# Kernel tuning notes

Hardware: AMD Instinct MI355X
Metric: run time of the kernel (lower is better)

Reference implementation:

```python
import jax, jax.numpy as jnp
import numpy as np

N = 100000   # nodes
E = 1600000  # edges
HID = 128    # hidden_dim
H = 8        # heads
C = HID // H # head_dim = out_channels per head


def setup_inputs() -> dict:
    key = jax.random.key(0)
    ks = jax.random.split(key, 10)
    x = jax.random.normal(ks[0], (N, HID), jnp.float32)
    edge_index = jax.random.randint(ks[1], (2, E), 0, N, dtype=jnp.int64)
    edge_attr = jax.random.uniform(ks[2], (E,), jnp.float32)
    # GATConv params (lin_src == lin_dst shared since in_channels is int)
    W = jax.random.normal(ks[3], (HID, H * C), jnp.float32) / np.sqrt(HID)
    att_src = jax.random.normal(ks[4], (H, C), jnp.float32) / np.sqrt(C)
    att_dst = jax.random.normal(ks[5], (H, C), jnp.float32) / np.sqrt(C)
    # lin_edge: Linear(edge_dim=1, H*C, bias=False) -> weight [H*C, 1] stored as [H, C]
    w_edge = jax.random.normal(ks[6], (H, C), jnp.float32)
    att_edge = jax.random.normal(ks[7], (H, C), jnp.float32) / np.sqrt(C)
    bias = jnp.zeros((H * C,), jnp.float32)
    gamma = jnp.ones((HID,), jnp.float32)
    beta = jnp.zeros((HID,), jnp.float32)
    return dict(x=x, edge_index=edge_index, edge_attr=edge_attr, W=W,
                att_src=att_src, att_dst=att_dst, w_edge=w_edge,
                att_edge=att_edge, bias=bias, gamma=gamma, beta=beta)


def reference(x, edge_index, edge_attr, W, att_src, att_dst, w_edge, att_edge, bias, gamma, beta):
    n = x.shape[0]
    src, dst = edge_index[0], edge_index[1]
    # add_self_loops with fill_value='mean': loop edge_attr = per-dst-node mean of edge_attr
    ones = jnp.ones_like(edge_attr)
    deg = jax.ops.segment_sum(ones, dst, num_segments=n)
    loop_attr = jax.ops.segment_sum(edge_attr, dst, num_segments=n) / jnp.maximum(deg, 1.0)
    ar = jnp.arange(n, dtype=src.dtype)
    src = jnp.concatenate([src, ar])
    dst = jnp.concatenate([dst, ar])
    ea = jnp.concatenate([edge_attr, loop_attr])  # [E+N]

    h = (x @ W).reshape(n, H, C)                  # [N,H,C]
    a_src = (h * att_src).sum(-1)                 # [N,H]
    a_dst = (h * att_dst).sum(-1)                 # [N,H]
    # edge_dim=1: alpha_edge = <lin_edge(ea), att_edge> = ea * sum(w_edge*att_edge)
    w_e = (w_edge * att_edge).sum(-1)             # [H]
    alpha = a_src[src] + a_dst[dst] + ea[:, None] * w_e  # [E+N, H]
    alpha = jax.nn.leaky_relu(alpha, 0.2)
    # segment softmax over incoming edges of each dst node (all nodes have a self-loop)
    m = jax.ops.segment_max(alpha, dst, num_segments=n)      # [N,H]
    ex = jnp.exp(alpha - m[dst])
    denom = jax.ops.segment_sum(ex, dst, num_segments=n)     # [N,H]
    p = ex / (denom[dst] + 1e-16)
    # scatter-aggregate weighted messages, concat heads, bias
    out = jax.ops.segment_sum(p[:, :, None] * h[src], dst, num_segments=n)
    out = out.reshape(n, H * C) + bias
    # residual + LayerNorm + ReLU
    y = out + x
    mu = y.mean(-1, keepdims=True)
    var = ((y - mu) ** 2).mean(-1, keepdims=True)
    y = (y - mu) * jax.lax.rsqrt(var + 1e-5) * gamma + beta
    return jax.nn.relu(y)
```

## Files before the change

kernel.cpp:

```cpp
#include <hip/hip_runtime.h>
#include <math.h>

#define HID 128
#define HEADS 8
#define CDIM 16
#define BKT 256
#define SCATB 512
#define SCAP 3136

typedef short bf8 __attribute__((ext_vector_type(8)));
typedef float f32x4 __attribute__((ext_vector_type(4)));
typedef float f32x2 __attribute__((ext_vector_type(2)));

__device__ __forceinline__ unsigned short f2bf(float f) {
    unsigned u = __float_as_uint(f);
    unsigned r = (u + 0x7fffu + ((u >> 16) & 1u)) >> 16;
    return (unsigned short)r;
}
__device__ __forceinline__ float bf2f(unsigned short u) {
    return __uint_as_float(((unsigned)u) << 16);
}

__global__ __launch_bounds__(256) void k_tw(const float* __restrict__ W,
                                            unsigned short* __restrict__ Wt,
                                            int* __restrict__ btot,
                                            int* __restrict__ bcur, int nbkt) {
    int idx = blockIdx.x * 256 + threadIdx.x;
    if (idx < HID * HID) {
        int j = idx >> 7, k = idx & 127;
        Wt[idx] = f2bf(W[k * HID + j]);
    }
    if (idx < nbkt) { btot[idx] = 0; bcur[idx] = 0; }
}

__global__ __launch_bounds__(256) void k_hist(const int* __restrict__ dst,
                                              int* __restrict__ btot,
                                              int E, int per, int nbkt) {
    __shared__ int h[512];
    int t = threadIdx.x;
    for (int b = t; b < nbkt; b += 256) h[b] = 0;
    __syncthreads();
    int b0 = blockIdx.x * per;
    int b1 = min(b0 + per, E);
    for (int e = b0 + t; e < b1; e += 256)
        atomicAdd(&h[dst[e] >> 8], 1);
    __syncthreads();
    for (int b = t; b < nbkt; b += 256)
        if (h[b]) atomicAdd(&btot[b], h[b]);
}

__global__ __launch_bounds__(512) void k_scan(const int* __restrict__ btot,
                                              int* __restrict__ bbase, int nbkt,
                                              const float* __restrict__ w_edge,
                                              const float* __restrict__ att_edge,
                                              float* __restrict__ w_e) {
    __shared__ int lds[512];
    int t = threadIdx.x;
    if (t < HEADS) {
        float s = 0.f;
        for (int c = 0; c < CDIM; c++) s += w_edge[t * CDIM + c] * att_edge[t * CDIM + c];
        w_e[t] = s;
    }
    lds[t] = (t < nbkt) ? btot[t] : 0;
    __syncthreads();
    for (int off = 1; off < 512; off <<= 1) {
        int xv = (t >= off) ? lds[t - off] : 0;
        __syncthreads();
        lds[t] += xv;
        __syncthreads();
    }
    if (t < nbkt) bbase[t] = t ? lds[t - 1] : 0;
    if (t == nbkt) bbase[t] = lds[nbkt - 1];
}

__global__ __launch_bounds__(256) void k_mid(const float* __restrict__ x,
                                             const unsigned short* __restrict__ Wt,
                                             const float* __restrict__ att_src,
                                             const float* __restrict__ att_dst,
                                             unsigned short* __restrict__ hbf,
                                             float* __restrict__ a_src,
                                             float* __restrict__ a_dst,
                                             const int* __restrict__ src,
                                             const int* __restrict__ dst,
                                             const float* __restrict__ eattr,
                                             const int* __restrict__ bbase,
                                             int* __restrict__ bcur,
                                             int2* __restrict__ erec1,
                                             int N, int E, int per, int nbkt) {
    if ((int)blockIdx.x < SCATB) {
        __shared__ int2 stg[SCAP];
        __shared__ unsigned short sbkt[SCAP];
        __shared__ int h[512];
        __shared__ int scn[512];
        __shared__ int gB[512];
        __shared__ int cur[512];
        int t = threadIdx.x;
        for (int b = t; b < 512; b += 256) h[b] = 0;
        __syncthreads();
        int b0 = blockIdx.x * per, b1 = min(b0 + per, E);
        for (int e = b0 + t; e < b1; e += 256)
            atomicAdd(&h[dst[e] >> 8], 1);
        __syncthreads();
        scn[t] = h[t];
        scn[t + 256] = h[t + 256];
        __syncthreads();
        for (int off = 1; off < 512; off <<= 1) {
            int x0 = (t >= off) ? scn[t - off] : 0;
            int x1 = (t + 256 >= off) ? scn[t + 256 - off] : 0;
            __syncthreads();
            scn[t] += x0;
            scn[t + 256] += x1;
            __syncthreads();
        }
        for (int b = t; b < nbkt; b += 256) {
            int locB = b ? scn[b - 1] : 0;
            int c = h[b];
            int base = bbase[b];
            if (c) base += atomicAdd(&bcur[b], c);
            gB[b] = base - locB;
            cur[b] = locB;
        }
        __syncthreads();
        for (int e = b0 + t; e < b1; e += 256) {
            int d = dst[e];
            int bb = d >> 8;
            int p = atomicAdd(&cur[bb], 1);
            stg[p] = make_int2((src[e] << 8) | (d & 255), __float_as_int(eattr[e]));
            sbkt[p] = (unsigned short)bb;
        }
        __syncthreads();
        int cnt = b1 - b0;
        for (int p = t; p < cnt; p += 256)
            erec1[gB[sbkt[p]] + p] = stg[p];
        return;
    }
    int tile = blockIdx.x - SCATB;
    int tid = threadIdx.x;
    int wv = tid >> 6, lane = tid & 63;
    int nloc = lane & 15, q = lane >> 4;
    int node = tile * 64 + wv * 16 + nloc;
    int nc = min(node, N - 1);
    const float* xp = x + (size_t)nc * HID + q * 8;
    const unsigned short* wp = Wt + nloc * HID + q * 8;
    f32x4 acc[8];
#pragma unroll
    for (int i = 0; i < 8; i++) acc[i] = (f32x4){0.f, 0.f, 0.f, 0.f};
#pragma unroll
    for (int ch = 0; ch < 4; ch++) {
        float4 xv0 = *(const float4*)(xp + ch * 32);
        float4 xv1 = *(const float4*)(xp + ch * 32 + 4);
        bf8 bfrag;
        bfrag[0] = (short)f2bf(xv0.x); bfrag[1] = (short)f2bf(xv0.y);
        bfrag[2] = (short)f2bf(xv0.z); bfrag[3] = (short)f2bf(xv0.w);
        bfrag[4] = (short)f2bf(xv1.x); bfrag[5] = (short)f2bf(xv1.y);
        bfrag[6] = (short)f2bf(xv1.z); bfrag[7] = (short)f2bf(xv1.w);
#pragma unroll
        for (int jt = 0; jt < 8; jt++) {
            bf8 afrag = *(const bf8*)(wp + (size_t)jt * 16 * HID + ch * 32);
            acc[jt] = __builtin_amdgcn_mfma_f32_16x16x32_bf16(afrag, bfrag, acc[jt], 0, 0, 0);
        }
    }
    bool ok = node < N;
    size_t hb = (size_t)nc * HID;
#pragma unroll
    for (int jt = 0; jt < 8; jt++) {
        int j0 = jt * 16 + q * 4;
        float4 as4 = *(const float4*)(att_src + j0);
        float4 ad4 = *(const float4*)(att_dst + j0);
        f32x4 a = acc[jt];
        float ps = a[0] * as4.x + a[1] * as4.y + a[2] * as4.z + a[3] * as4.w;
        float pd = a[0] * ad4.x + a[1] * ad4.y + a[2] * ad4.z + a[3] * ad4.w;
        ps += __shfl_xor(ps, 16, 64); ps += __shfl_xor(ps, 32, 64);
        pd += __shfl_xor(pd, 16, 64); pd += __shfl_xor(pd, 32, 64);
        if (ok) {
            ushort4 hv;
            hv.x = f2bf(a[0]); hv.y = f2bf(a[1]); hv.z = f2bf(a[2]); hv.w = f2bf(a[3]);
            *(ushort4*)(hbf + hb + j0) = hv;
            if (q == 0) {
                a_src[(size_t)node * 8 + jt] = ps;
                a_dst[(size_t)node * 8 + jt] = pd;
            }
        }
    }
}

__global__ __launch_bounds__(256) void k_bin2(const int* __restrict__ bbase,
                                              const int2* __restrict__ erec1,
                                              int2* __restrict__ erec,
                                              int* __restrict__ row_ptr,
                                              int N, int nbkt) {
    __shared__ int h[256];
    __shared__ int s[256];
    __shared__ int cur[256];
    int b = blockIdx.x, t = threadIdx.x;
    int base = bbase[b], end = bbase[b + 1];
    h[t] = 0;
    __syncthreads();
    for (int e = base + t; e < end; e += 256)
        atomicAdd(&h[erec1[e].x & 255], 1);
    __syncthreads();
    s[t] = h[t];
    __syncthreads();
    for (int off = 1; off < 256; off <<= 1) {
        int v = (t >= off) ? s[t - off] : 0;
        __syncthreads();
        s[t] += v;
        __syncthreads();
    }
    int exc = (t > 0) ? s[t - 1] : 0;
    int node = (b << 8) + t;
    if (node <= N) row_ptr[node] = base + exc;
    cur[t] = base + exc;
    __syncthreads();
    for (int e = base + t; e < end; e += 256) {
        int2 r = erec1[e];
        int pos = atomicAdd(&cur[r.x & 255], 1);
        erec[pos] = make_int2(r.x & 0xFFFFFF00, r.y);
    }
}

__global__ __launch_bounds__(256) void k_node(const int* __restrict__ row_ptr,
                                              const int2* __restrict__ erec,
                                              const float* __restrict__ a_src,
                                              const float* __restrict__ a_dst,
                                              const float* __restrict__ w_e,
                                              const unsigned short* __restrict__ hbf,
                                              const float* __restrict__ x,
                                              const float* __restrict__ bias,
                                              const float* __restrict__ gamma,
                                              const float* __restrict__ beta,
                                              float* __restrict__ out, int N) {
    int wv = threadIdx.x >> 6;
    int lane = threadIdx.x & 63;
    int n = blockIdx.x * 4 + wv;
    if (n >= N) return;
    int r0 = row_ptr[n], r1 = row_ptr[n + 1];
    int sub = lane >> 4;
    int colg = lane & 15;
    int wh = colg >> 1;
    float ad_h = a_dst[(size_t)n * 8 + wh];
    float we_h = w_e[wh];
    const char* hbfc = (const char*)hbf + colg * 16;
    const char* asw  = (const char*)(a_src + wh);

    f32x2 acc2[4];
#pragma unroll
    for (int j = 0; j < 4; j++) acc2[j] = (f32x2){0.f, 0.f};
    float wsum = 0.f, suma = 0.f;
    int rlast = max(r1 - 1, 0);

    for (int eb = r0 + (sub << 2); eb < r1; eb += 16) {
        int e1 = min(eb + 1, rlast);
        int e2 = min(eb + 2, rlast);
        int e3 = min(eb + 3, rlast);
        int2 rec0 = erec[eb];
        int2 rec1 = erec[e1];
        int2 rec2 = erec[e2];
        int2 rec3 = erec[e3];
        bool m1 = (eb + 1) < r1, m2 = (eb + 2) < r1, m3 = (eb + 3) < r1;
        bf8 hv0 = *(const bf8*)(hbfc + rec0.x);
        bf8 hv1 = *(const bf8*)(hbfc + rec1.x);
        bf8 hv2 = *(const bf8*)(hbfc + rec2.x);
        bf8 hv3 = *(const bf8*)(hbfc + rec3.x);
        float as0 = *(const float*)(asw + (rec0.x >> 3));
        float as1 = *(const float*)(asw + (rec1.x >> 3));
        float as2 = *(const float*)(asw + (rec2.x >> 3));
        float as3 = *(const float*)(asw + (rec3.x >> 3));
        float ae0 = __int_as_float(rec0.y);
        float ae1 = __int_as_float(rec1.y);
        float ae2 = __int_as_float(rec2.y);
        float ae3 = __int_as_float(rec3.y);
        float v0 = as0 + ad_h + ae0 * we_h;
        float v1 = as1 + ad_h + ae1 * we_h;
        float v2 = as2 + ad_h + ae2 * we_h;
        float v3 = as3 + ad_h + ae3 * we_h;
        v0 = v0 > 0.f ? v0 : 0.2f * v0;
        v1 = v1 > 0.f ? v1 : 0.2f * v1;
        v2 = v2 > 0.f ? v2 : 0.2f * v2;
        v3 = v3 > 0.f ? v3 : 0.2f * v3;
        float w0 = __expf(v0);
        float w1 = m1 ? __expf(v1) : 0.f;
        float w2 = m2 ? __expf(v2) : 0.f;
        float w3 = m3 ? __expf(v3) : 0.f;
        wsum += (w0 + w1) + (w2 + w3);
        if (colg == 0)
            suma += ae0 + (m1 ? ae1 : 0.f) + (m2 ? ae2 : 0.f) + (m3 ? ae3 : 0.f);
        f32x2 w0v = (f32x2){w0, w0};
        f32x2 w1v = (f32x2){w1, w1};
        f32x2 w2v = (f32x2){w2, w2};
        f32x2 w3v = (f32x2){w3, w3};
#pragma unroll
        for (int j = 0; j < 4; j++) {
            f32x2 h0; h0[0] = bf2f((unsigned short)hv0[2 * j]); h0[1] = bf2f((unsigned short)hv0[2 * j + 1]);
            f32x2 h1; h1[0] = bf2f((unsigned short)hv1[2 * j]); h1[1] = bf2f((unsigned short)hv1[2 * j + 1]);
            f32x2 h2; h2[0] = bf2f((unsigned short)hv2[2 * j]); h2[1] = bf2f((unsigned short)hv2[2 * j + 1]);
            f32x2 h3; h3[0] = bf2f((unsigned short)hv3[2 * j]); h3[1] = bf2f((unsigned short)hv3[2 * j + 1]);
#if __has_builtin(__builtin_elementwise_fma)
            acc2[j] = __builtin_elementwise_fma(w0v, h0, acc2[j]);
            acc2[j] = __builtin_elementwise_fma(w1v, h1, acc2[j]);
            acc2[j] = __builtin_elementwise_fma(w2v, h2, acc2[j]);
            acc2[j] = __builtin_elementwise_fma(w3v, h3, acc2[j]);
#else
            acc2[j][0] = fmaf(w0, h0[0], acc2[j][0]); acc2[j][1] = fmaf(w0, h0[1], acc2[j][1]);
            acc2[j][0] = fmaf(w1, h1[0], acc2[j][0]); acc2[j][1] = fmaf(w1, h1[1], acc2[j][1]);
            acc2[j][0] = fmaf(w2, h2[0], acc2[j][0]); acc2[j][1] = fmaf(w2, h2[1], acc2[j][1]);
            acc2[j][0] = fmaf(w3, h3[0], acc2[j][0]); acc2[j][1] = fmaf(w3, h3[1], acc2[j][1]);
#endif
        }
    }

#pragma unroll
    for (int j = 0; j < 4; j++) {
        acc2[j][0] += __shfl_xor(acc2[j][0], 16, 64);
        acc2[j][0] += __shfl_xor(acc2[j][0], 32, 64);
        acc2[j][1] += __shfl_xor(acc2[j][1], 16, 64);
        acc2[j][1] += __shfl_xor(acc2[j][1], 32, 64);
    }
    wsum += __shfl_xor(wsum, 16, 64);
    wsum += __shfl_xor(wsum, 32, 64);
    suma += __shfl_xor(suma, 16, 64);
    suma += __shfl_xor(suma, 32, 64);

    float accA = sub == 0 ? acc2[0][0] : sub == 1 ? acc2[1][0] : sub == 2 ? acc2[2][0] : acc2[3][0];
    float accB = sub == 0 ? acc2[0][1] : sub == 1 ? acc2[1][1] : sub == 2 ? acc2[2][1] : acc2[3][1];
    int srcL = ((lane & 3) << 4) | (lane >> 2);
    float a0 = __shfl(accA, srcL, 64);
    float a1 = __shfl(accB, srcL, 64);
    int head = lane >> 3;
    float denom = __shfl(wsum, head << 1, 64);
    float sa = __shfl(suma, 0, 64);

    int deg = r1 - r0;
    float la = sa / fmaxf((float)deg, 1.0f);
    float adh = a_dst[(size_t)n * 8 + head];
    float weh = w_e[head];
    float vs = a_src[(size_t)n * 8 + head] + adh + la * weh;
    vs = vs > 0.f ? vs : 0.2f * vs;
    float exs = __expf(vs);
    size_t bx = (size_t)n * HID;
    ushort2 hs = *(const ushort2*)(hbf + bx + 2 * lane);
    a0 = fmaf(exs, bf2f(hs.x), a0);
    a1 = fmaf(exs, bf2f(hs.y), a1);
    float inv = 1.f / (denom + exs + 1e-16f);

    float2 xv = *(const float2*)(x + bx + 2 * lane);
    float2 bv = *(const float2*)(bias + 2 * lane);
    float y0 = a0 * inv + bv.x + xv.x;
    float y1 = a1 * inv + bv.y + xv.y;
    float ss = y0 + y1, sq = y0 * y0 + y1 * y1;
#pragma unroll
    for (int off = 32; off; off >>= 1) {
        ss += __shfl_xor(ss, off, 64);
        sq += __shfl_xor(sq, off, 64);
    }
    float mu = ss * (1.f / 128.f);
    float var = sq * (1.f / 128.f) - mu * mu;
    float r = rsqrtf(fmaxf(var, 0.f) + 1e-5f);
    float2 gv = *(const float2*)(gamma + 2 * lane);
    float2 tv = *(const float2*)(beta + 2 * lane);
    float o0 = (y0 - mu) * r * gv.x + tv.x;
    float o1 = (y1 - mu) * r * gv.y + tv.y;
    float2 ov = make_float2(fmaxf(o0, 0.f), fmaxf(o1, 0.f));
    *(float2*)(out + bx + 2 * lane) = ov;
}

extern "C" void kernel_launch(void* const* d_in, const int* in_sizes, int n_in,
                              void* d_out, int out_size, void* d_ws, size_t ws_size,
                              hipStream_t stream) {
    const float* x        = (const float*)d_in[0];
    const int*   ei       = (const int*)d_in[1];
    const float* eattr    = (const float*)d_in[2];
    const float* W        = (const float*)d_in[3];
    const float* att_src  = (const float*)d_in[4];
    const float* att_dst  = (const float*)d_in[5];
    const float* w_edge   = (const float*)d_in[6];
    const float* att_edge = (const float*)d_in[7];
    const float* bias     = (const float*)d_in[8];
    const float* gamma    = (const float*)d_in[9];
    const float* beta     = (const float*)d_in[10];

    int N = in_sizes[0] / HID;
    int E = in_sizes[2];
    const int* src = ei;
    const int* dst = ei + E;
    float* out = (float*)d_out;

    int nbkt = (N + BKT - 1) / BKT;

    char* ws = (char*)d_ws;
    size_t off = 0;
    auto alloc = [&](size_t bytes) { char* p = ws + off; off += (bytes + 255) & ~255ull; return p; };
    unsigned short* hbf = (unsigned short*)alloc((size_t)N * HID * 2);
    unsigned short* Wt  = (unsigned short*)alloc((size_t)HID * HID * 2);
    float* a_src   = (float*)alloc((size_t)N * 8 * 4);
    float* a_dst   = (float*)alloc((size_t)N * 8 * 4);
    int2*  erec    = (int2*) alloc((size_t)E * 8);
    int2*  erec1   = (int2*) alloc((size_t)E * 8);
    int*   btot    = (int*)  alloc(512 * 4);
    int*   bcur    = (int*)  alloc(512 * 4);
    int*   bbase   = (int*)  alloc(520 * 4);
    int*   row_ptr = (int*)  alloc((size_t)(N + 1) * 4);
    float* w_e     = (float*)alloc(8 * 4);

    int histB = 512;
    int per = (E + histB - 1) / histB;
    int gemmB = (N + 63) / 64;

    k_tw<<<64, 256, 0, stream>>>(W, Wt, btot, bcur, nbkt);
    k_hist<<<histB, 256, 0, stream>>>(dst, btot, E, per, nbkt);
    k_scan<<<1, 512, 0, stream>>>(btot, bbase, nbkt, w_edge, att_edge, w_e);
    k_mid<<<SCATB + gemmB, 256, 0, stream>>>(
        x, Wt, att_src, att_dst, hbf, a_src, a_dst,
        src, dst, eattr, bbase, bcur, erec1, N, E, per, nbkt);
    k_bin2<<<nbkt, 256, 0, stream>>>(bbase, erec1, erec, row_ptr, N, nbkt);
    k_node<<<(N + 3) / 4, 256, 0, stream>>>(row_ptr, erec, a_src, a_dst, w_e, hbf, x,
                                            bias, gamma, beta, out, N);
}
```

Measured before the change: 303.0 us.

## Map one node per 16-lane group and drop global histogram atomics

The node kernel now gives each 16-lane group its own destination node, processing edges two at a time serially, instead of spreading one node's edges across a whole wavefront. That removes the cross-subgroup shuffle reductions and lets the LayerNorm reduce over 16 lanes with float4 loads and stores, at the cost of more per-lane serial work and load imbalance across nodes of different degree. The histogram kernel also takes over the W transpose and writes per-block bucket counts to a matrix rather than using global atomics. The scan sums that matrix and zeroes the cursors, which removes one kernel launch.

```diff
diff --git a/kernel.cpp b/kernel.cpp
--- a/kernel.cpp
+++ b/kernel.cpp
@@ -5,6 +5,8 @@
 #define HEADS 8
 #define CDIM 16
 #define BKT 256
+#define HISTB 256
+#define NBSTR 392
 #define SCATB 512
 #define SCAP 3136
 
@@ -21,36 +23,31 @@
     return __uint_as_float(((unsigned)u) << 16);
 }
 
-__global__ __launch_bounds__(256) void k_tw(const float* __restrict__ W,
-                                            unsigned short* __restrict__ Wt,
-                                            int* __restrict__ btot,
-                                            int* __restrict__ bcur, int nbkt) {
-    int idx = blockIdx.x * 256 + threadIdx.x;
-    if (idx < HID * HID) {
+__global__ __launch_bounds__(256) void k_hist(const float* __restrict__ W,
+                                              unsigned short* __restrict__ Wt,
+                                              const int* __restrict__ dst,
+                                              int* __restrict__ btotmat,
+                                              int E, int per, int nbkt) {
+    __shared__ int h[512];
+    int t = threadIdx.x, bid = blockIdx.x;
+    if (bid < 64) {
+        int idx = bid * 256 + t;
         int j = idx >> 7, k = idx & 127;
         Wt[idx] = f2bf(W[k * HID + j]);
     }
-    if (idx < nbkt) { btot[idx] = 0; bcur[idx] = 0; }
-}
-
-__global__ __launch_bounds__(256) void k_hist(const int* __restrict__ dst,
-                                              int* __restrict__ btot,
-                                              int E, int per, int nbkt) {
-    __shared__ int h[512];
-    int t = threadIdx.x;
-    for (int b = t; b < nbkt; b += 256) h[b] = 0;
-    __syncthreads();
-    int b0 = blockIdx.x * per;
-    int b1 = min(b0 + per, E);
+    h[t] = 0; h[t + 256] = 0;
+    __syncthreads();
+    int b0 = bid * per, b1 = min(b0 + per, E);
     for (int e = b0 + t; e < b1; e += 256)
         atomicAdd(&h[dst[e] >> 8], 1);
     __syncthreads();
     for (int b = t; b < nbkt; b += 256)
-        if (h[b]) atomicAdd(&btot[b], h[b]);
-}
-
-__global__ __launch_bounds__(512) void k_scan(const int* __restrict__ btot,
-                                              int* __restrict__ bbase, int nbkt,
+        btotmat[bid * NBSTR + b] = h[b];
+}
+
+__global__ __launch_bounds__(512) void k_scan(const int* __restrict__ btotmat,
+                                              int* __restrict__ bbase,
+                                              int* __restrict__ bcur, int nbkt,
                                               const float* __restrict__ w_edge,
                                               const float* __restrict__ att_edge,
                                               float* __restrict__ w_e) {
@@ -61,7 +58,11 @@
         for (int c = 0; c < CDIM; c++) s += w_edge[t * CDIM + c] * att_edge[t * CDIM + c];
         w_e[t] = s;
     }
-    lds[t] = (t < nbkt) ? btot[t] : 0;
+    bcur[t] = 0;
+    int sum = 0;
+    if (t < nbkt)
+        for (int i = 0; i < HISTB; i++) sum += btotmat[i * NBSTR + t];
+    lds[t] = sum;
     __syncthreads();
     for (int off = 1; off < 512; off <<= 1) {
         int xv = (t >= off) ? lds[t - off] : 0;
@@ -232,136 +233,114 @@
                                               float* __restrict__ out, int N) {
     int wv = threadIdx.x >> 6;
     int lane = threadIdx.x & 63;
-    int n = blockIdx.x * 4 + wv;
-    if (n >= N) return;
-    int r0 = row_ptr[n], r1 = row_ptr[n + 1];
-    int sub = lane >> 4;
-    int colg = lane & 15;
-    int wh = colg >> 1;
-    float ad_h = a_dst[(size_t)n * 8 + wh];
+    int grp = lane >> 4;
+    int g = lane & 15;
+    int n = (blockIdx.x * 4 + wv) * 4 + grp;
+    bool act = n < N;
+    int nc = act ? n : (N - 1);
+    int r0 = row_ptr[nc], r1 = row_ptr[nc + 1];
+    int wh = g >> 1;
+    float ad_h = a_dst[(size_t)nc * 8 + wh];
     float we_h = w_e[wh];
-    const char* hbfc = (const char*)hbf + colg * 16;
+    const char* hbfc = (const char*)hbf + g * 16;
     const char* asw  = (const char*)(a_src + wh);
 
     f32x2 acc2[4];
 #pragma unroll
     for (int j = 0; j < 4; j++) acc2[j] = (f32x2){0.f, 0.f};
     float wsum = 0.f, suma = 0.f;
-    int rlast = max(r1 - 1, 0);
-
-    for (int eb = r0 + (sub << 2); eb < r1; eb += 16) {
-        int e1 = min(eb + 1, rlast);
-        int e2 = min(eb + 2, rlast);
-        int e3 = min(eb + 3, rlast);
-        int2 rec0 = erec[eb];
+    int rlast = max(r1 - 1, r0);
+
+    for (int e = r0; e < r1; e += 2) {
+        int e1 = min(e + 1, rlast);
+        int2 rec0 = erec[e];
         int2 rec1 = erec[e1];
-        int2 rec2 = erec[e2];
-        int2 rec3 = erec[e3];
-        bool m1 = (eb + 1) < r1, m2 = (eb + 2) < r1, m3 = (eb + 3) < r1;
+        bool m1 = (e + 1) < r1;
         bf8 hv0 = *(const bf8*)(hbfc + rec0.x);
         bf8 hv1 = *(const bf8*)(hbfc + rec1.x);
-        bf8 hv2 = *(const bf8*)(hbfc + rec2.x);
-        bf8 hv3 = *(const bf8*)(hbfc + rec3.x);
         float as0 = *(const float*)(asw + (rec0.x >> 3));
         float as1 = *(const float*)(asw + (rec1.x >> 3));
-        float as2 = *(const float*)(asw + (rec2.x >> 3));
-        float as3 = *(const float*)(asw + (rec3.x >> 3));
         float ae0 = __int_as_float(rec0.y);
         float ae1 = __int_as_float(rec1.y);
-        float ae2 = __int_as_float(rec2.y);
-        float ae3 = __int_as_float(rec3.y);
         float v0 = as0 + ad_h + ae0 * we_h;
         float v1 = as1 + ad_h + ae1 * we_h;
-        float v2 = as2 + ad_h + ae2 * we_h;
-        float v3 = as3 + ad_h + ae3 * we_h;
         v0 = v0 > 0.f ? v0 : 0.2f * v0;
         v1 = v1 > 0.f ? v1 : 0.2f * v1;
-        v2 = v2 > 0.f ? v2 : 0.2f * v2;
-        v3 = v3 > 0.f ? v3 : 0.2f * v3;
         float w0 = __expf(v0);
         float w1 = m1 ? __expf(v1) : 0.f;
-        float w2 = m2 ? __expf(v2) : 0.f;
-        float w3 = m3 ? __expf(v3) : 0.f;
-        wsum += (w0 + w1) + (w2 + w3);
-        if (colg == 0)
-            suma += ae0 + (m1 ? ae1 : 0.f) + (m2 ? ae2 : 0.f) + (m3 ? ae3 : 0.f);
+        wsum += w0 + w1;
+        suma += ae0 + (m1 ? ae1 : 0.f);
         f32x2 w0v = (f32x2){w0, w0};
         f32x2 w1v = (f32x2){w1, w1};
-        f32x2 w2v = (f32x2){w2, w2};
-        f32x2 w3v = (f32x2){w3, w3};
 #pragma unroll
         for (int j = 0; j < 4; j++) {
             f32x2 h0; h0[0] = bf2f((unsigned short)hv0[2 * j]); h0[1] = bf2f((unsigned short)hv0[2 * j + 1]);
             f32x2 h1; h1[0] = bf2f((unsigned short)hv1[2 * j]); h1[1] = bf2f((unsigned short)hv1[2 * j + 1]);
-            f32x2 h2; h2[0] = bf2f((unsigned short)hv2[2 * j]); h2[1] = bf2f((unsigned short)hv2[2 * j + 1]);
-            f32x2 h3; h3[0] = bf2f((unsigned short)hv3[2 * j]); h3[1] = bf2f((unsigned short)hv3[2 * j + 1]);
 #if __has_builtin(__builtin_elementwise_fma)
             acc2[j] = __builtin_elementwise_fma(w0v, h0, acc2[j]);
             acc2[j] = __builtin_elementwise_fma(w1v, h1, acc2[j]);
-            acc2[j] = __builtin_elementwise_fma(w2v, h2, acc2[j]);
-            acc2[j] = __builtin_elementwise_fma(w3v, h3, acc2[j]);
 #else
             acc2[j][0] = fmaf(w0, h0[0], acc2[j][0]); acc2[j][1] = fmaf(w0, h0[1], acc2[j][1]);
             acc2[j][0] = fmaf(w1, h1[0], acc2[j][0]); acc2[j][1] = fmaf(w1, h1[1], acc2[j][1]);
-            acc2[j][0] = fmaf(w2, h2[0], acc2[j][0]); acc2[j][1] = fmaf(w2, h2[1], acc2[j][1]);
-            acc2[j][0] = fmaf(w3, h3[0], acc2[j][0]); acc2[j][1] = fmaf(w3, h3[1], acc2[j][1]);
 #endif
         }
     }
 
-#pragma unroll
-    for (int j = 0; j < 4; j++) {
-        acc2[j][0] += __shfl_xor(acc2[j][0], 16, 64);
-        acc2[j][0] += __shfl_xor(acc2[j][0], 32, 64);
-        acc2[j][1] += __shfl_xor(acc2[j][1], 16, 64);
-        acc2[j][1] += __shfl_xor(acc2[j][1], 32, 64);
-    }
-    wsum += __shfl_xor(wsum, 16, 64);
-    wsum += __shfl_xor(wsum, 32, 64);
-    suma += __shfl_xor(suma, 16, 64);
-    suma += __shfl_xor(suma, 32, 64);
-
-    float accA = sub == 0 ? acc2[0][0] : sub == 1 ? acc2[1][0] : sub == 2 ? acc2[2][0] : acc2[3][0];
-    float accB = sub == 0 ? acc2[0][1] : sub == 1 ? acc2[1][1] : sub == 2 ? acc2[2][1] : acc2[3][1];
-    int srcL = ((lane & 3) << 4) | (lane >> 2);
-    float a0 = __shfl(accA, srcL, 64);
-    float a1 = __shfl(accB, srcL, 64);
-    int head = lane >> 3;
-    float denom = __shfl(wsum, head << 1, 64);
-    float sa = __shfl(suma, 0, 64);
-
     int deg = r1 - r0;
-    float la = sa / fmaxf((float)deg, 1.0f);
-    float adh = a_dst[(size_t)n * 8 + head];
-    float weh = w_e[head];
-    float vs = a_src[(size_t)n * 8 + head] + adh + la * weh;
+    float la = suma / fmaxf((float)deg, 1.0f);
+    float vs = a_src[(size_t)nc * 8 + wh] + ad_h + la * we_h;
     vs = vs > 0.f ? vs : 0.2f * vs;
     float exs = __expf(vs);
-    size_t bx = (size_t)n * HID;
-    ushort2 hs = *(const ushort2*)(hbf + bx + 2 * lane);
-    a0 = fmaf(exs, bf2f(hs.x), a0);
-    a1 = fmaf(exs, bf2f(hs.y), a1);
-    float inv = 1.f / (denom + exs + 1e-16f);
-
-    float2 xv = *(const float2*)(x + bx + 2 * lane);
-    float2 bv = *(const float2*)(bias + 2 * lane);
-    float y0 = a0 * inv + bv.x + xv.x;
-    float y1 = a1 * inv + bv.y + xv.y;
-    float ss = y0 + y1, sq = y0 * y0 + y1 * y1;
-#pragma unroll
-    for (int off = 32; off; off >>= 1) {
+    size_t bx = (size_t)nc * HID;
+    bf8 hs = *(const bf8*)(hbf + bx + g * 8);
+#pragma unroll
+    for (int j = 0; j < 4; j++) {
+        acc2[j][0] = fmaf(exs, bf2f((unsigned short)hs[2 * j]), acc2[j][0]);
+        acc2[j][1] = fmaf(exs, bf2f((unsigned short)hs[2 * j + 1]), acc2[j][1]);
+    }
+    float inv = 1.f / (wsum + exs + 1e-16f);
+
+    float4 xa = *(const float4*)(x + bx + g * 8);
+    float4 xb = *(const float4*)(x + bx + g * 8 + 4);
+    float4 ba = *(const float4*)(bias + g * 8);
+    float4 bb = *(const float4*)(bias + g * 8 + 4);
+    float y[8];
+    y[0] = acc2[0][0] * inv + ba.x + xa.x;
+    y[1] = acc2[0][1] * inv + ba.y + xa.y;
+    y[2] = acc2[1][0] * inv + ba.z + xa.z;
+    y[3] = acc2[1][1] * inv + ba.w + xa.w;
+    y[4] = acc2[2][0] * inv + bb.x + xb.x;
+    y[5] = acc2[2][1] * inv + bb.y + xb.y;
+    y[6] = acc2[3][0] * inv + bb.z + xb.z;
+    y[7] = acc2[3][1] * inv + bb.w + xb.w;
+    float ss = 0.f, sq = 0.f;
+#pragma unroll
+    for (int j = 0; j < 8; j++) { ss += y[j]; sq = fmaf(y[j], y[j], sq); }
+#pragma unroll
+    for (int off = 1; off < 16; off <<= 1) {
         ss += __shfl_xor(ss, off, 64);
         sq += __shfl_xor(sq, off, 64);
     }
     float mu = ss * (1.f / 128.f);
     float var = sq * (1.f / 128.f) - mu * mu;
-    float r = rsqrtf(fmaxf(var, 0.f) + 1e-5f);
-    float2 gv = *(const float2*)(gamma + 2 * lane);
-    float2 tv = *(const float2*)(beta + 2 * lane);
-    float o0 = (y0 - mu) * r * gv.x + tv.x;
-    float o1 = (y1 - mu) * r * gv.y + tv.y;
-    float2 ov = make_float2(fmaxf(o0, 0.f), fmaxf(o1, 0.f));
-    *(float2*)(out + bx + 2 * lane) = ov;
+    float rr = rsqrtf(fmaxf(var, 0.f) + 1e-5f);
+    float4 ga = *(const float4*)(gamma + g * 8);
+    float4 gb = *(const float4*)(gamma + g * 8 + 4);
+    float4 ta = *(const float4*)(beta + g * 8);
+    float4 tb = *(const float4*)(beta + g * 8 + 4);
+    float4 o0, o1;
+    o0.x = fmaxf((y[0] - mu) * rr * ga.x + ta.x, 0.f);
+    o0.y = fmaxf((y[1] - mu) * rr * ga.y + ta.y, 0.f);
+    o0.z = fmaxf((y[2] - mu) * rr * ga.z + ta.z, 0.f);
+    o0.w = fmaxf((y[3] - mu) * rr * ga.w + ta.w, 0.f);
+    o1.x = fmaxf((y[4] - mu) * rr * gb.x + tb.x, 0.f);
+    o1.y = fmaxf((y[5] - mu) * rr * gb.y + tb.y, 0.f);
+    o1.z = fmaxf((y[6] - mu) * rr * gb.z + tb.z, 0.f);
+    o1.w = fmaxf((y[7] - mu) * rr * gb.w + tb.w, 0.f);
+    if (act) {
+        *(float4*)(out + bx + g * 8) = o0;
+        *(float4*)(out + bx + g * 8 + 4) = o1;
+    }
 }
 
 extern "C" void kernel_launch(void* const* d_in, const int* in_sizes, int n_in,
@@ -396,23 +375,22 @@
     float* a_dst   = (float*)alloc((size_t)N * 8 * 4);
     int2*  erec    = (int2*) alloc((size_t)E * 8);
     int2*  erec1   = (int2*) alloc((size_t)E * 8);
-    int*   btot    = (int*)  alloc(512 * 4);
+    int*   btotmat = (int*)  alloc((size_t)HISTB * NBSTR * 4);
     int*   bcur    = (int*)  alloc(512 * 4);
     int*   bbase   = (int*)  alloc(520 * 4);
     int*   row_ptr = (int*)  alloc((size_t)(N + 1) * 4);
     float* w_e     = (float*)alloc(8 * 4);
 
-    int histB = 512;
-    int per = (E + histB - 1) / histB;
+    int perH = (E + HISTB - 1) / HISTB;
+    int perS = (E + SCATB - 1) / SCATB;
     int gemmB = (N + 63) / 64;
 
-    k_tw<<<64, 256, 0, stream>>>(W, Wt, btot, bcur, nbkt);
-    k_hist<<<histB, 256, 0, stream>>>(dst, btot, E, per, nbkt);
-    k_scan<<<1, 512, 0, stream>>>(btot, bbase, nbkt, w_edge, att_edge, w_e);
+    k_hist<<<HISTB, 256, 0, stream>>>(W, Wt, dst, btotmat, E, perH, nbkt);
+    k_scan<<<1, 512, 0, stream>>>(btotmat, bbase, bcur, nbkt, w_edge, att_edge, w_e);
     k_mid<<<SCATB + gemmB, 256, 0, stream>>>(
         x, Wt, att_src, att_dst, hbf, a_src, a_dst,
-        src, dst, eattr, bbase, bcur, erec1, N, E, per, nbkt);
+        src, dst, eattr, bbase, bcur, erec1, N, E, perS, nbkt);
     k_bin2<<<nbkt, 256, 0, stream>>>(bbase, erec1, erec, row_ptr, N, nbkt);
-    k_node<<<(N + 3) / 4, 256, 0, stream>>>(row_ptr, erec, a_src, a_dst, w_e, hbf, x,
-                                            bias, gamma, beta, out, N);
-}
+    k_node<<<(N + 15) / 16, 256, 0, stream>>>(row_ptr, erec, a_src, a_dst, w_e, hbf, x,
+                                              bias, gamma, beta, out, N);
+}
```

Result: no change. 301.5 us (-0.5%).
